# Performance work log

Hardware: AMD Instinct MI355X
Metric: run time of the kernel (lower is better)

Reference implementation:

```python
import jax, jax.numpy as jnp
import numpy as np

B, T, D, H = 4, 2048, 1024, 16
HD = D // H  # head_dim = 64

def setup_inputs() -> dict:
    key = jax.random.key(0)
    k1, k2, k3 = jax.random.split(key, 3)
    s = 1.0 / np.sqrt(D)
    x = jax.random.normal(k1, (B, T, D), dtype=jnp.float32)
    W_qkv = jax.random.normal(k2, (D, 3 * D), dtype=jnp.float32) * s
    W_proj = jax.random.normal(k3, (D, D), dtype=jnp.float32) * s
    return {"x": x, "W_qkv": W_qkv, "W_proj": W_proj}

def reference(x, W_qkv, W_proj):
    Bq, Tq, C = x.shape
    qkv = x @ W_qkv                                   # [B,T,3C]
    q, k, v = jnp.split(qkv, 3, axis=-1)
    def heads(t):  # [B,T,C] -> [B,H,T,HD]
        return t.reshape(Bq, Tq, H, HD).transpose(0, 2, 1, 3)
    q, k, v = heads(q), heads(k), heads(v)
    scale = 1.0 / np.sqrt(HD)
    att = jnp.einsum('bhqd,bhkd->bhqk', q, k) * scale  # [B,H,T,T]
    causal = jnp.tril(jnp.ones((Tq, Tq), dtype=bool))
    att = jnp.where(causal[None, None], att, -jnp.inf)
    att = jax.nn.softmax(att, axis=-1)
    y = jnp.einsum('bhqk,bhkd->bhqd', att, v)          # [B,H,T,HD]
    y = y.transpose(0, 2, 1, 3).reshape(Bq, Tq, C)
    return y @ W_proj
```

## Files before the change

kernel.cpp:

```cpp
#include <hip/hip_runtime.h>

typedef unsigned short ushort_t;
typedef __attribute__((ext_vector_type(8))) __bf16 bf16x8;
typedef __attribute__((ext_vector_type(4))) float f32x4;
typedef __attribute__((ext_vector_type(16))) float f32x16;
typedef __attribute__((ext_vector_type(4))) float float4v;
typedef __attribute__((ext_vector_type(8))) unsigned short ushort8v;
typedef __attribute__((ext_vector_type(4))) unsigned short ushort4v;
typedef __attribute__((ext_vector_type(4))) unsigned uint4v;

#define T_LEN 2048
#define D_DIM 1024
#define NHEAD 16
#define HDIM 64
#define BH 64
#define MROWS 8192
#define PERQKV ((size_t)BH * T_LEN * HDIM)

__device__ __forceinline__ ushort_t f2bf(float f) {
  unsigned u = __builtin_bit_cast(unsigned, f);
  u = (u + 0x7FFFu + ((u >> 16) & 1u)) >> 16;
  return (ushort_t)u;
}

__device__ __forceinline__ float fast_exp2(float x) {
  float r; asm("v_exp_f32 %0, %1" : "=v"(r) : "v"(x)); return r;
}

__device__ __forceinline__ void load_lds16(const ushort_t* g, ushort_t* l) {
  __builtin_amdgcn_global_load_lds((const __attribute__((address_space(1))) void*)g,
                                   (__attribute__((address_space(3))) void*)l, 16, 0, 0);
}

__global__ __launch_bounds__(256) void k_cvt_x(const float* __restrict__ x,
                                               ushort_t* __restrict__ xb) {
  int i = blockIdx.x * 256 + threadIdx.x;
  float4v v = ((const float4v*)x)[i];
  ushort4v o;
  o[0] = f2bf(v[0]); o[1] = f2bf(v[1]); o[2] = f2bf(v[2]); o[3] = f2bf(v[3]);
  ((ushort4v*)xb)[i] = o;
}

__global__ __launch_bounds__(256) void k_transpose(const float* __restrict__ W,
                                                   ushort_t* __restrict__ Wt,
                                                   int R, int C) {
  __shared__ ushort_t tile[32][33];
  int tx = threadIdx.x & 31, ty = threadIdx.x >> 5;
  int r0 = blockIdx.y << 5, c0 = blockIdx.x << 5;
#pragma unroll
  for (int i = 0; i < 4; ++i) {
    int r = ty + i * 8;
    tile[r][tx] = f2bf(W[(size_t)(r0 + r) * C + c0 + tx]);
  }
  __syncthreads();
#pragma unroll
  for (int i = 0; i < 4; ++i) {
    int r = ty + i * 8;
    Wt[(size_t)(c0 + r) * R + r0 + tx] = tile[tx][r];
  }
}

template <int NB_TILES, int EPI>
__global__ __launch_bounds__(512, 2) void k_gemm3(const ushort_t* __restrict__ A,
                                                  const ushort_t* __restrict__ Bt,
                                                  ushort_t* __restrict__ O16,
                                                  float* __restrict__ O32) {
  __shared__ __align__(16) ushort_t As[3][128 * 64];
  __shared__ __align__(16) ushort_t Bs[3][256 * 64];
  const int tid = threadIdx.x, lane = tid & 63, w = tid >> 6;
  const int g = lane >> 4, c = lane & 15;
  const int wm = w & 1, wn = w >> 1;
  const int nblk = 64 * NB_TILES;
  const int chunk = nblk >> 3;
  const int bid = blockIdx.x;
  const int logical = (bid & 7) * chunk + (bid >> 3);
  const int mb = logical & 63, nb = logical >> 6;
  const int m0 = mb * 128, n0 = nb * 256;

  const int srow = lane >> 3, sgran = lane & 7;

  auto stage = [&](int t, int buf) {
    const int k0 = t * 64;
#pragma unroll
    for (int l = 0; l < 2; ++l) {
      int r = w * 16 + l * 8 + srow;
      load_lds16(A + (size_t)(m0 + r) * 1024 + k0 + ((sgran ^ (r & 7)) << 3),
                 &As[buf][(w * 16 + l * 8) * 64]);
    }
#pragma unroll
    for (int l = 0; l < 4; ++l) {
      int r = w * 32 + l * 8 + srow;
      load_lds16(Bt + (size_t)(n0 + r) * 1024 + k0 + ((sgran ^ (r & 7)) << 3),
                 &Bs[buf][(w * 32 + l * 8) * 64]);
    }
  };

  f32x4 acc[4][4];
#pragma unroll
  for (int i = 0; i < 4; ++i)
#pragma unroll
    for (int j = 0; j < 4; ++j) acc[i][j] = (f32x4){0.f, 0.f, 0.f, 0.f};

  stage(0, 0);
  stage(1, 1);

  for (int t = 0; t < 16; ++t) {
    if (t < 15) asm volatile("s_waitcnt vmcnt(6)" ::: "memory");
    else        asm volatile("s_waitcnt vmcnt(0)" ::: "memory");
    __builtin_amdgcn_s_barrier();
    __builtin_amdgcn_sched_barrier(0);

    if (t + 2 < 16) stage(t + 2, (t + 2) % 3);

    const int cur = t % 3;
    const ushort_t* abuf = &As[cur][0];
    const ushort_t* bbuf = &Bs[cur][0];
#pragma unroll
    for (int kk = 0; kk < 2; ++kk) {
      bf16x8 af[4], bq[4];
#pragma unroll
      for (int fr = 0; fr < 4; ++fr) {
        int r = wm * 64 + fr * 16 + c;
        af[fr] = *(const bf16x8*)&abuf[r * 64 + (((kk * 4 + g) ^ (r & 7)) << 3)];
      }
#pragma unroll
      for (int fc = 0; fc < 4; ++fc) {
        int r = wn * 64 + fc * 16 + c;
        bq[fc] = *(const bf16x8*)&bbuf[r * 64 + (((kk * 4 + g) ^ (r & 7)) << 3)];
      }
      __builtin_amdgcn_s_setprio(1);
#pragma unroll
      for (int fr = 0; fr < 4; ++fr)
#pragma unroll
        for (int fc = 0; fc < 4; ++fc)
          acc[fr][fc] = __builtin_amdgcn_mfma_f32_16x16x32_bf16(af[fr], bq[fc],
                                                                acc[fr][fc], 0, 0, 0);
      __builtin_amdgcn_s_setprio(0);
    }
  }

#pragma unroll
  for (int fr = 0; fr < 4; ++fr)
#pragma unroll
    for (int fc = 0; fc < 4; ++fc) {
      int n = n0 + wn * 64 + fc * 16 + c;
#pragma unroll
      for (int j = 0; j < 4; ++j) {
        int m = m0 + wm * 64 + fr * 16 + g * 4 + j;
        float v = acc[fr][fc][j];
        if constexpr (EPI == 0) {
          int which = n >> 10, hn = n & 1023;
          int h = hn >> 6, d = hn & 63;
          int b = m >> 11, tt = m & 2047;
          if (which == 0) v *= 0.18033688f;
          O16[(size_t)which * PERQKV +
              (((size_t)(b * NHEAD + h) * T_LEN + tt) * HDIM + d)] = f2bf(v);
        } else {
          O32[(size_t)m * (64 * NB_TILES * 4) + n] = v;
        }
      }
    }
}

__global__ __launch_bounds__(128, 4) void k_attn(const ushort_t* __restrict__ Q,
                                                 const ushort_t* __restrict__ Kv,
                                                 const ushort_t* __restrict__ Vv,
                                                 ushort_t* __restrict__ Y) {
  __shared__ __align__(16) ushort_t Kt[2][64 * 64];
  __shared__ __align__(16) ushort_t Vt[2][64 * 64];

  const int bid = blockIdx.x;
  const int bh = (bid & 7) * 8 + ((bid >> 3) & 7);
  const int pairidx = bid >> 6;
  const int pA = 31 - pairidx, pB = pairidx;
  const int nktA = pA + 1;
  const int total = nktA + pB + 1;

  const int tid = threadIdx.x, lane = tid & 63, w = tid >> 6;
  const int hi = lane >> 5, lc = lane & 31;
  const size_t base = (size_t)bh * (T_LEN * HDIM);

  int q32 = pA * 64 + w * 32;
  bf16x8 qf[4];
#pragma unroll
  for (int st = 0; st < 4; ++st)
    qf[st] = *(const bf16x8*)(Q + base + (size_t)(q32 + lc) * HDIM + st * 16 + hi * 8);

  f32x16 o0, o1;
#pragma unroll
  for (int i = 0; i < 16; ++i) { o0[i] = 0.f; o1[i] = 0.f; }
  float mrun = 0.f, lrun = 0.f;

  const int ksl = tid & 7, krow0 = tid >> 3;
  const int kpair = tid & 31, vk0 = 2 * kpair, vd0 = (tid >> 5) * 8;

  bf16x8 kreg[4];
  ushort8v vreg[4];
  auto stage_issue = [&](int kt) {
    const ushort_t* kb = Kv + base + (size_t)kt * 64 * HDIM;
    const ushort_t* vb = Vv + base + (size_t)kt * 64 * HDIM;
    vreg[0] = *(const ushort8v*)(vb + (size_t)vk0 * HDIM + vd0);
    vreg[1] = *(const ushort8v*)(vb + (size_t)(vk0 + 1) * HDIM + vd0);
    vreg[2] = *(const ushort8v*)(vb + (size_t)vk0 * HDIM + vd0 + 32);
    vreg[3] = *(const ushort8v*)(vb + (size_t)(vk0 + 1) * HDIM + vd0 + 32);
#pragma unroll
    for (int m = 0; m < 4; ++m)
      kreg[m] = *(const bf16x8*)(kb + (size_t)(krow0 + 16 * m) * HDIM + ksl * 8);
  };
  auto stage_write = [&](int buf) {
#pragma unroll
    for (int m = 0; m < 4; ++m) {
      int r = krow0 + 16 * m;
      *(bf16x8*)&Kt[buf][r * 64 + ((ksl ^ (r & 7)) << 3)] = kreg[m];
    }
#pragma unroll
    for (int e = 0; e < 8; ++e) {
      int rd = vd0 + e;
      unsigned pv = (unsigned)vreg[0][e] | ((unsigned)vreg[1][e] << 16);
      *(unsigned*)&Vt[buf][rd * 64 + (((kpair >> 2) ^ (rd & 7)) << 3) + 2 * (kpair & 3)] = pv;
      int rd2 = rd + 32;
      unsigned pv2 = (unsigned)vreg[2][e] | ((unsigned)vreg[3][e] << 16);
      *(unsigned*)&Vt[buf][rd2 * 64 + (((kpair >> 2) ^ (rd2 & 7)) << 3) + 2 * (kpair & 3)] = pv2;
    }
  };

  const int b_ = bh >> 4, h_ = bh & 15;
  auto epilogue = [&]() {
    float lt = lrun + __shfl_xor(lrun, 32);
    float invl = 1.f / lt;
#pragma unroll
    for (int r = 0; r < 16; ++r) {
      int cr = (r & 3) + 8 * (r >> 2) + 4 * hi;
      float iv = __shfl(invl, cr);
      size_t m = (size_t)b_ * T_LEN + q32 + cr;
      Y[m * D_DIM + h_ * HDIM + lc]      = f2bf(o0[r] * iv);
      Y[m * D_DIM + h_ * HDIM + 32 + lc] = f2bf(o1[r] * iv);
    }
  };

  stage_issue(0); stage_write(0);
  stage_issue(1);
  __syncthreads();

  for (int it = 0; it < total; ++it) {
    if (it == nktA) {
      epilogue();
      q32 = pB * 64 + w * 32;
#pragma unroll
      for (int st = 0; st < 4; ++st)
        qf[st] = *(const bf16x8*)(Q + base + (size_t)(q32 + lc) * HDIM + st * 16 + hi * 8);
#pragma unroll
      for (int i = 0; i < 16; ++i) { o0[i] = 0.f; o1[i] = 0.f; }
      mrun = 0.f; lrun = 0.f;
    }
    const int kt = (it < nktA) ? it : it - nktA;
    const int cur = it & 1;
    const ushort_t* kbuf = &Kt[cur][0];
    const ushort_t* vbuf = &Vt[cur][0];

    f32x16 s0, s1;
#pragma unroll
    for (int i = 0; i < 16; ++i) { s0[i] = 0.f; s1[i] = 0.f; }
    __builtin_amdgcn_s_setprio(1);
#pragma unroll
    for (int st = 0; st < 4; ++st) {
      bf16x8 kf0 = *(const bf16x8*)&kbuf[lc * 64 + (((2 * st + hi) ^ (lc & 7)) << 3)];
      s0 = __builtin_amdgcn_mfma_f32_32x32x16_bf16(kf0, qf[st], s0, 0, 0, 0);
    }
#pragma unroll
    for (int st = 0; st < 4; ++st) {
      bf16x8 kf1 = *(const bf16x8*)&kbuf[(32 + lc) * 64 + (((2 * st + hi) ^ (lc & 7)) << 3)];
      s1 = __builtin_amdgcn_mfma_f32_32x32x16_bf16(kf1, qf[st], s1, 0, 0, 0);
    }
    __builtin_amdgcn_s_setprio(0);

    if (kt * 64 + 63 > q32) {
      const int q = q32 + lc;
#pragma unroll
      for (int r = 0; r < 16; ++r) {
        int cr = (r & 3) + 8 * (r >> 2) + 4 * hi;
        if (kt * 64 + cr > q)      s0[r] = -3.0e38f;
        if (kt * 64 + 32 + cr > q) s1[r] = -3.0e38f;
      }
    }

    float tm[8];
#pragma unroll
    for (int i = 0; i < 8; ++i) tm[i] = fmaxf(fmaxf(s0[i], s0[i + 8]), fmaxf(s1[i], s1[i + 8]));
#pragma unroll
    for (int i = 0; i < 4; ++i) tm[i] = fmaxf(tm[i], tm[i + 4]);
    float tmax = fmaxf(fmaxf(tm[0], tm[1]), fmaxf(tm[2], tm[3]));
    tmax = fmaxf(tmax, __shfl_xor(tmax, 32));

    if (!__all(tmax <= mrun + 11.0f)) {
      float mnew = fmaxf(mrun, tmax);
      float sc = fast_exp2(mrun - mnew);
      lrun *= sc; mrun = mnew;
#pragma unroll
      for (int r = 0; r < 16; ++r) {
        int cr = (r & 3) + 8 * (r >> 2) + 4 * hi;
        float scr = __shfl(sc, cr);
        o0[r] *= scr; o1[r] *= scr;
      }
    }

#pragma unroll
    for (int r = 0; r < 16; ++r) s0[r] = fast_exp2(s0[r] - mrun);
#pragma unroll
    for (int r = 0; r < 16; ++r) s1[r] = fast_exp2(s1[r] - mrun);
    {
      float u0 = 0.f, u1 = 0.f, u2 = 0.f, u3 = 0.f;
#pragma unroll
      for (int i = 0; i < 4; ++i) {
        u0 += s0[i];     u1 += s0[i + 4];  u2 += s0[i + 8];  u3 += s0[i + 12];
        u0 += s1[i];     u1 += s1[i + 4];  u2 += s1[i + 8];  u3 += s1[i + 12];
      }
      lrun += (u0 + u1) + (u2 + u3);
    }

    unsigned wv[16];
#pragma unroll
    for (int i = 0; i < 8; ++i) {
      asm("v_cvt_pk_bf16_f32 %0, %1, %2" : "=v"(wv[i])     : "v"(s0[2 * i]), "v"(s0[2 * i + 1]));
      asm("v_cvt_pk_bf16_f32 %0, %1, %2" : "=v"(wv[8 + i]) : "v"(s1[2 * i]), "v"(s1[2 * i + 1]));
    }
    bf16x8 pf[4];
#pragma unroll
    for (int g4 = 0; g4 < 4; ++g4) {
      unsigned a0 = wv[4 * g4], a1 = wv[4 * g4 + 1];
      unsigned a2 = wv[4 * g4 + 2], a3 = wv[4 * g4 + 3];
      asm("v_permlane32_swap_b32 %0, %1" : "+v"(a0), "+v"(a2));
      asm("v_permlane32_swap_b32 %0, %1" : "+v"(a1), "+v"(a3));
      uint4v fw; fw[0] = a0; fw[1] = a1; fw[2] = a2; fw[3] = a3;
      pf[g4] = __builtin_bit_cast(bf16x8, fw);
    }

    __builtin_amdgcn_s_setprio(1);
#pragma unroll
    for (int km = 0; km < 4; ++km) {
      int gsl = ((2 * km + hi) ^ (lc & 7)) << 3;
      bf16x8 vb0 = *(const bf16x8*)&vbuf[lc * 64 + gsl];
      bf16x8 vb1 = *(const bf16x8*)&vbuf[(32 + lc) * 64 + gsl];
      o0 = __builtin_amdgcn_mfma_f32_32x32x16_bf16(pf[km], vb0, o0, 0, 0, 0);
      o1 = __builtin_amdgcn_mfma_f32_32x32x16_bf16(pf[km], vb1, o1, 0, 0, 0);
    }
    __builtin_amdgcn_s_setprio(0);

    if (it + 1 < total) stage_write((it + 1) & 1);
    if (it + 2 < total) {
      int itn = it + 2;
      stage_issue((itn < nktA) ? itn : itn - nktA);
    }
    __syncthreads();
  }

  epilogue();
}

extern "C" void kernel_launch(void* const* d_in, const int* in_sizes, int n_in,
                              void* d_out, int out_size, void* d_ws, size_t ws_size,
                              hipStream_t stream) {
  const float* x     = (const float*)d_in[0];
  const float* Wqkv  = (const float*)d_in[1];
  const float* Wproj = (const float*)d_in[2];
  float* out = (float*)d_out;
  ushort_t* ws = (ushort_t*)d_ws;

  ushort_t* Xb  = ws;
  ushort_t* WqT = Xb  + (size_t)MROWS * D_DIM;
  ushort_t* WpT = WqT + (size_t)3 * D_DIM * D_DIM;
  ushort_t* Qb  = WpT + (size_t)D_DIM * D_DIM;
  ushort_t* Kb  = Qb + PERQKV;
  ushort_t* Vb  = Kb + PERQKV;
  ushort_t* Yb  = Vb + PERQKV;

  k_cvt_x<<<(MROWS * D_DIM / 4) / 256, 256, 0, stream>>>(x, Xb);
  k_transpose<<<dim3(3 * D_DIM / 32, D_DIM / 32), 256, 0, stream>>>(Wqkv, WqT, D_DIM, 3 * D_DIM);
  k_transpose<<<dim3(D_DIM / 32, D_DIM / 32), 256, 0, stream>>>(Wproj, WpT, D_DIM, D_DIM);
  k_gemm3<12, 0><<<768, 512, 0, stream>>>(Xb, WqT, Qb, nullptr);
  k_attn<<<1024, 128, 0, stream>>>(Qb, Kb, Vb, Yb);
  k_gemm3<4, 1><<<256, 512, 0, stream>>>(Yb, WpT, nullptr, out);
}
```

Measured before the change: 195.6 us.

## Replace QKV projection GEMM with simpler single-buffered 128x128 tile kernel

Adds a new templated GEMM kernel using 128x128 output tiles, K-step 32, 256 threads and single-buffered swizzled LDS tiles, and uses it for the QKV projection in place of the triple-buffered 128x256 k_gemm3 kernel. The simpler kernel drops the multi-stage prefetch pipeline in favour of lower LDS use and possibly higher occupancy. It risks exposing global-load latency because the loads are no longer overlapped with MFMA work, and it re-reads inputs more often because the tiles are smaller.

```diff
diff --git a/kernel.cpp b/kernel.cpp
--- a/kernel.cpp
+++ b/kernel.cpp
@@ -58,6 +58,83 @@
     int r = ty + i * 8;
     Wt[(size_t)(c0 + r) * R + r0 + tx] = tile[tx][r];
   }
+}
+
+template <int N, int K, int EPI>
+__global__ __launch_bounds__(256) void k_gemm(const ushort_t* __restrict__ A,
+                                              const ushort_t* __restrict__ Bt,
+                                              ushort_t* __restrict__ O16,
+                                              float* __restrict__ O32) {
+  __shared__ __align__(16) ushort_t Atile[128 * 32];
+  __shared__ __align__(16) ushort_t Btile[128 * 32];
+  const int tid = threadIdx.x;
+  const int lane = tid & 63, w = tid >> 6;
+  const int g = lane >> 4, c = lane & 15;
+  const int wm = w >> 1, wn = w & 1;
+  const int m0 = blockIdx.y * 128, n0 = blockIdx.x * 128;
+
+  f32x4 acc[4][4];
+#pragma unroll
+  for (int i = 0; i < 4; ++i)
+#pragma unroll
+    for (int j = 0; j < 4; ++j) acc[i][j] = (f32x4){0.f, 0.f, 0.f, 0.f};
+
+  for (int k0 = 0; k0 < K; k0 += 32) {
+    __syncthreads();
+#pragma unroll
+    for (int r = 0; r < 2; ++r) {
+      int flat = r * 256 + tid;
+      int row = flat >> 2, slot = flat & 3;
+      int gsl = slot ^ (row & 3);
+      load_lds16(A + (size_t)(m0 + row) * K + k0 + gsl * 8,
+                 &Atile[(r * 256 + w * 64) * 8]);
+      load_lds16(Bt + (size_t)(n0 + row) * K + k0 + gsl * 8,
+                 &Btile[(r * 256 + w * 64) * 8]);
+    }
+    __syncthreads();
+
+    bf16x8 af[4], bfr[4];
+#pragma unroll
+    for (int mi = 0; mi < 4; ++mi) {
+      int row = wm * 64 + mi * 16 + c;
+      int sl = g ^ (row & 3);
+      af[mi] = *(const bf16x8*)&Atile[row * 32 + sl * 8];
+    }
+#pragma unroll
+    for (int ni = 0; ni < 4; ++ni) {
+      int row = wn * 64 + ni * 16 + c;
+      int sl = g ^ (row & 3);
+      bfr[ni] = *(const bf16x8*)&Btile[row * 32 + sl * 8];
+    }
+#pragma unroll
+    for (int mi = 0; mi < 4; ++mi)
+#pragma unroll
+      for (int ni = 0; ni < 4; ++ni)
+        acc[mi][ni] = __builtin_amdgcn_mfma_f32_16x16x32_bf16(af[mi], bfr[ni],
+                                                              acc[mi][ni], 0, 0, 0);
+  }
+
+#pragma unroll
+  for (int mi = 0; mi < 4; ++mi)
+#pragma unroll
+    for (int ni = 0; ni < 4; ++ni) {
+      int n = n0 + wn * 64 + ni * 16 + c;
+#pragma unroll
+      for (int j = 0; j < 4; ++j) {
+        int m = m0 + wm * 64 + mi * 16 + g * 4 + j;
+        float v = acc[mi][ni][j];
+        if constexpr (EPI == 0) {
+          int which = n >> 10, hn = n & 1023;
+          int h = hn >> 6, d = hn & 63;
+          int b = m >> 11, t = m & 2047;
+          if (which == 0) v *= 0.18033688f;
+          O16[(size_t)which * PERQKV +
+              (((size_t)(b * NHEAD + h) * T_LEN + t) * HDIM + d)] = f2bf(v);
+        } else {
+          O32[(size_t)m * N + n] = v;
+        }
+      }
+    }
 }
 
 template <int NB_TILES, int EPI>
@@ -377,7 +454,7 @@
   k_cvt_x<<<(MROWS * D_DIM / 4) / 256, 256, 0, stream>>>(x, Xb);
   k_transpose<<<dim3(3 * D_DIM / 32, D_DIM / 32), 256, 0, stream>>>(Wqkv, WqT, D_DIM, 3 * D_DIM);
   k_transpose<<<dim3(D_DIM / 32, D_DIM / 32), 256, 0, stream>>>(Wproj, WpT, D_DIM, D_DIM);
-  k_gemm3<12, 0><<<768, 512, 0, stream>>>(Xb, WqT, Qb, nullptr);
+  k_gemm<3 * D_DIM, D_DIM, 0><<<dim3(3 * D_DIM / 128, MROWS / 128), 256, 0, stream>>>(Xb, WqT, Qb, nullptr);
   k_attn<<<1024, 128, 0, stream>>>(Qb, Kb, Vb, Yb);
   k_gemm3<4, 1><<<256, 512, 0, stream>>>(Yb, WpT, nullptr, out);
 }
```

Result: faster. 186.0 us (-4.9%).
